# Kernel optimization log

Measured on AMD Instinct MI355X. Metric: run time of the kernel, lower is better.

## Reference

```python
import jax, jax.numpy as jnp
import numpy as np

H = 256
K = 16
EPS_LN = 1e-5


def setup_inputs() -> dict:
    key = jax.random.key(0)
    ks = jax.random.split(key, 24)
    B, N = 64, 256
    s = lambda *sh: 1.0 / np.sqrt(sh[0])
    inp = {
        "feat": jax.random.normal(ks[0], (B, N, H), jnp.float32),
        "centers": jax.random.normal(ks[1], (B, N, 3), jnp.float32),
        "text_global": jax.random.normal(ks[2], (B, H), jnp.float32),
        # geom_mlp: Linear(4,H) -> ReLU -> Linear(H,H) -> ReLU
        "w_geom1": jax.random.normal(ks[3], (4, H), jnp.float32) * s(4),
        "b_geom1": jnp.zeros((H,), jnp.float32),
        "w_geom2": jax.random.normal(ks[4], (H, H), jnp.float32) * s(H),
        "b_geom2": jnp.zeros((H,), jnp.float32),
        # text gate / bias projections
        "w_gate": jax.random.normal(ks[5], (H, H), jnp.float32) * s(H),
        "b_gate": jnp.zeros((H,), jnp.float32),
        "w_tbias": jax.random.normal(ks[6], (H, H), jnp.float32) * s(H),
        "b_tbias": jnp.zeros((H,), jnp.float32),
        # edge_mlp: Linear(H,H//2) -> ReLU -> Linear(H//2,1)
        "w_edge1": jax.random.normal(ks[7], (H, H // 2), jnp.float32) * s(H),
        "b_edge1": jnp.zeros((H // 2,), jnp.float32),
        "w_edge2": jax.random.normal(ks[8], (H // 2, 1), jnp.float32) * s(H // 2),
        "b_edge2": jnp.zeros((1,), jnp.float32),
        # msg_mlp: Linear(H,H) -> ReLU
        "w_msg": jax.random.normal(ks[9], (H, H), jnp.float32) * s(H),
        "b_msg": jnp.zeros((H,), jnp.float32),
        # out_proj: Linear(2H,H) -> ReLU
        "w_out": jax.random.normal(ks[10], (2 * H, H), jnp.float32) * s(2 * H),
        "b_out": jnp.zeros((H,), jnp.float32),
        # LayerNorm params
        "ln_gamma": jnp.ones((H,), jnp.float32),
        "ln_beta": jnp.zeros((H,), jnp.float32),
    }
    return inp


def _forward(feat, centers, text_global,
             w_geom1, b_geom1, w_geom2, b_geom2,
             w_gate, b_gate, w_tbias, b_tbias,
             w_edge1, b_edge1, w_edge2, b_edge2,
             w_msg, b_msg, w_out, b_out, ln_gamma, ln_beta):
    B, N, Hd = feat.shape
    k = min(K, N)
    # pairwise euclidean distances (B,N,N)
    sq = jnp.sum(centers * centers, axis=-1)  # (B,N)
    d2 = sq[:, :, None] + sq[:, None, :] - 2.0 * jnp.einsum('bnc,bmc->bnm', centers, centers)
    dist_matrix = jnp.sqrt(jnp.maximum(d2, 0.0))
    # k smallest -> top_k of negated distances (sorted ascending in distance)
    _, knn_idx = jax.lax.top_k(-dist_matrix, k)  # (B,N,k)
    idx_flat = knn_idx.reshape(B, N * k)
    feat_neigh = jnp.take_along_axis(feat, idx_flat[:, :, None], axis=1).reshape(B, N, k, Hd)
    centers_neigh = jnp.take_along_axis(centers, idx_flat[:, :, None], axis=1).reshape(B, N, k, 3)
    rel = centers_neigh - centers[:, :, None, :]  # (B,N,k,3)
    dist = jnp.linalg.norm(rel, axis=-1, keepdims=True) + 1e-6
    geom = jnp.concatenate([rel, jnp.log1p(dist)], axis=-1)  # (B,N,k,4)
    geom_emb = jax.nn.relu(jax.nn.relu(geom @ w_geom1 + b_geom1) @ w_geom2 + b_geom2)
    text_gate = jax.nn.sigmoid(text_global @ w_gate + b_gate)[:, None, None, :]
    text_bias = (text_global @ w_tbias + b_tbias)[:, None, None, :]
    geom_cond = geom_emb * text_gate + text_bias
    edge_feat = jnp.tanh(feat[:, :, None, :] + feat_neigh + geom_cond)  # (B,N,k,H)
    edge_logits = (jax.nn.relu(edge_feat @ w_edge1 + b_edge1) @ w_edge2 + b_edge2)[..., 0]
    edge_alpha = jax.nn.softmax(edge_logits, axis=-1)[..., None]  # (B,N,k,1)
    msg = jax.nn.relu(feat_neigh @ w_msg + b_msg)
    ctx = jnp.sum(edge_alpha * msg, axis=2)  # (B,N,H)
    out = jax.nn.relu(jnp.concatenate([feat, ctx], axis=-1) @ w_out + b_out)
    x = feat + out
    mu = jnp.mean(x, axis=-1, keepdims=True)
    var = jnp.mean((x - mu) ** 2, axis=-1, keepdims=True)
    return (x - mu) / jnp.sqrt(var + EPS_LN) * ln_gamma + ln_beta


def reference(feat, centers, text_global,
              w_geom1, b_geom1, w_geom2, b_geom2,
              w_gate, b_gate, w_tbias, b_tbias,
              w_edge1, b_edge1, w_edge2, b_edge2,
              w_msg, b_msg, w_out, b_out, ln_gamma, ln_beta):
    return _forward(feat, centers, text_global,
                    w_geom1, b_geom1, w_geom2, b_geom2,
                    w_gate, b_gate, w_tbias, b_tbias,
                    w_edge1, b_edge1, w_edge2, b_edge2,
                    w_msg, b_msg, w_out, b_out, ln_gamma, ln_beta)
```

## Files before the change

kernel.cpp:

```cpp
#include <hip/hip_runtime.h>
#include <hip/hip_bf16.h>

#define H 256
#define KNN 16
#define NPT 256
#define BB 64

typedef unsigned short u16;
typedef unsigned int u32;
typedef __attribute__((ext_vector_type(8))) short shortx8;
typedef __attribute__((ext_vector_type(4))) float floatx4;

__device__ __forceinline__ u16 f2b(float f) {
    return __builtin_bit_cast(u16, __float2bfloat16(f));
}
__device__ __forceinline__ float b2f(u16 u) {
    return __uint_as_float(((u32)u) << 16);
}

__device__ __forceinline__ float fast_tanh(float x) {
    float e = __builtin_amdgcn_exp2f(x * 2.88539008177793f);
    return 1.0f - 2.0f * __builtin_amdgcn_rcpf(e + 1.0f);
}

__global__ __launch_bounds__(256) void prep_kernel(
    const float* __restrict__ w2, const float* __restrict__ we1,
    const float* __restrict__ wm, const float* __restrict__ wo,
    const float* __restrict__ w1, const float* __restrict__ b1,
    u16* __restrict__ w2t, u16* __restrict__ we1t,
    u16* __restrict__ wmt, u16* __restrict__ wot, u16* __restrict__ w1t) {
    int tid = blockIdx.x * 256 + threadIdx.x;
    if (tid < 65536) {
        int n = tid >> 8, k = tid & 255;
        w2t[tid] = f2b(w2[k * 256 + n]);
    } else if (tid < 98304) {
        int t = tid - 65536;
        int n = t >> 8, k = t & 255;
        we1t[t] = f2b(we1[k * 128 + n]);
    } else if (tid < 163840) {
        int t = tid - 98304;
        int n = t >> 8, k = t & 255;
        wmt[t] = f2b(wm[k * 256 + n]);
    } else if (tid < 294912) {
        int t = tid - 163840;
        int n = t >> 9, k = t & 511;
        wot[t] = f2b(wo[k * 256 + n]);
    } else {
        int t = tid - 294912;
        int n = t >> 5, k = t & 31;
        float v = (k < 4) ? w1[k * 256 + n] : (k == 4 ? b1[n] : 0.0f);
        w1t[t] = f2b(v);
    }
}

__global__ __launch_bounds__(256) void knn_kernel(const float* __restrict__ centers,
                                                  int* __restrict__ knn) {
    __shared__ float cx[NPT], cy[NPT], cz[NPT], sq[NPT];
    __shared__ float dl[4][64][17];
    __shared__ int il[4][64][17];
    int blk = blockIdx.x;
    int b = blk >> 2, n0 = (blk & 3) * 64;
    int h = threadIdx.x;
    int s = h >> 6, pt = h & 63;
    {
        const float* cb = centers + (size_t)b * NPT * 3;
        float x = cb[h * 3 + 0], y = cb[h * 3 + 1], z = cb[h * 3 + 2];
        cx[h] = x; cy[h] = y; cz[h] = z;
        sq[h] = x * x + y * y + z * z;
    }
    __syncthreads();
    int n = n0 + pt;
    float x = cx[n], y = cy[n], z = cz[n], sn = sq[n];
    float bd[KNN];
    int bi[KNN];
#pragma unroll
    for (int j = 0; j < KNN; j++) { bd[j] = 1e30f; bi[j] = 0x7fffffff; }
    for (int mm = 0; mm < 64; mm++) {
        int m = s * 64 + mm;
        float dot = x * cx[m] + y * cy[m] + z * cz[m];
        float d2 = (sn + sq[m]) - 2.0f * dot;
        float d = sqrtf(fmaxf(d2, 0.0f));
        if (d < bd[KNN - 1]) {
            bd[KNN - 1] = d; bi[KNN - 1] = m;
#pragma unroll
            for (int p = KNN - 1; p > 0; --p) {
                if (bd[p - 1] > bd[p]) {
                    float td = bd[p - 1]; bd[p - 1] = bd[p]; bd[p] = td;
                    int ti = bi[p - 1]; bi[p - 1] = bi[p]; bi[p] = ti;
                }
            }
        }
    }
#pragma unroll
    for (int j = 0; j < KNN; j++) { dl[s][pt][j] = bd[j]; il[s][pt][j] = bi[j]; }
    __syncthreads();
    if (s == 0) {
        float md[KNN];
        int mi[KNN];
#pragma unroll
        for (int j = 0; j < KNN; j++) { md[j] = dl[0][pt][j]; mi[j] = il[0][pt][j]; }
        for (int t = 1; t < 4; t++) {
            for (int j = 0; j < KNN; j++) {
                float d = dl[t][pt][j];
                int idx = il[t][pt][j];
                bool ins = (d < md[KNN - 1]) || (d == md[KNN - 1] && idx < mi[KNN - 1]);
                if (!ins) break;
                md[KNN - 1] = d; mi[KNN - 1] = idx;
#pragma unroll
                for (int p = KNN - 1; p > 0; --p) {
                    bool sw = (md[p - 1] > md[p]) ||
                              (md[p - 1] == md[p] && mi[p - 1] > mi[p]);
                    if (sw) {
                        float td = md[p - 1]; md[p - 1] = md[p]; md[p] = td;
                        int ti = mi[p - 1]; mi[p - 1] = mi[p]; mi[p] = ti;
                    }
                }
            }
        }
        int* kp = knn + (b * NPT + n0 + pt) * KNN;
#pragma unroll
        for (int j = 0; j < KNN; j++) kp[j] = mi[j];
    }
}

__global__ __launch_bounds__(1024) void gate_kernel(const float* __restrict__ tg_g,
                                                    const float* __restrict__ wg,
                                                    const float* __restrict__ bg,
                                                    const float* __restrict__ wtb,
                                                    const float* __restrict__ btb,
                                                    float* __restrict__ gate,
                                                    float* __restrict__ tbias) {
    __shared__ float tg[H];
    __shared__ float red[1024];
    int b = blockIdx.x, t = threadIdx.x;
    if (t < H) tg[t] = tg_g[b * H + t];
    __syncthreads();
    int o = t & 511;
    int half = t >> 9;
    int h = o & 255;
    const float* wsel = (o < 256) ? wg : wtb;
    float a = 0.0f;
#pragma unroll 4
    for (int i = half * 128; i < half * 128 + 128; i++)
        a += tg[i] * wsel[i * H + h];
    red[t] = a;
    __syncthreads();
    if (t < 512) {
        float s = red[t] + red[t + 512];
        if (o < 256) {
            gate[b * H + h] = 1.0f / (1.0f + expf(-(s + bg[h])));
        } else {
            tbias[b * H + h] = s + btb[h];
        }
    }
}

__global__ __launch_bounds__(256, 4) void msg_mfma(const float* __restrict__ feat,
                                                   const u16* __restrict__ wmt,
                                                   const float* __restrict__ bm,
                                                   u16* __restrict__ MSGB) {
    __shared__ __attribute__((aligned(16))) u16 A[64][264];
    int p0 = blockIdx.x * 64, h = threadIdx.x;
    int w = h >> 6, lane = h & 63, quad = lane >> 4, lq = lane & 15;
#pragma unroll 8
    for (int row = 0; row < 64; row++)
        A[row][h] = f2b(feat[(size_t)(p0 + row) * H + h]);
    __syncthreads();
    floatx4 acc[4][4];
#pragma unroll
    for (int rt = 0; rt < 4; rt++)
#pragma unroll
        for (int ct = 0; ct < 4; ct++) acc[rt][ct] = (floatx4){0, 0, 0, 0};
#pragma unroll 2
    for (int kt = 0; kt < 8; kt++) {
        shortx8 bf[4];
#pragma unroll
        for (int ct = 0; ct < 4; ct++)
            bf[ct] = *(const shortx8*)&wmt[(w * 64 + ct * 16 + lq) * 256 + kt * 32 + quad * 8];
#pragma unroll
        for (int rt = 0; rt < 4; rt++) {
            shortx8 a = *(const shortx8*)&A[rt * 16 + lq][kt * 32 + quad * 8];
#pragma unroll
            for (int ct = 0; ct < 4; ct++)
                acc[rt][ct] = __builtin_amdgcn_mfma_f32_16x16x32_bf16(a, bf[ct], acc[rt][ct], 0, 0, 0);
        }
    }
#pragma unroll
    for (int ct = 0; ct < 4; ct++) {
        int col = w * 64 + ct * 16 + lq;
        float bmc = bm[col];
#pragma unroll
        for (int rt = 0; rt < 4; rt++)
#pragma unroll
            for (int r = 0; r < 4; r++) {
                int row = rt * 16 + quad * 4 + r;
                MSGB[(size_t)(p0 + row) * H + col] = f2b(fmaxf(acc[rt][ct][r] + bmc, 0.0f));
            }
    }
}

__global__ __launch_bounds__(256, 4) void edge_mfma(
    const float* __restrict__ feat,
    const float* __restrict__ centers,
    const u16* __restrict__ w1t,
    const u16* __restrict__ w2t, const float* __restrict__ b2v,
    const u16* __restrict__ we1t, const float* __restrict__ be1,
    const float* __restrict__ we2, const float* __restrict__ be2,
    const int* __restrict__ knn, const float* __restrict__ gateG,
    const float* __restrict__ tbiasG, const u16* __restrict__ MSGB,
    u16* __restrict__ ctxB) {
    __shared__ __attribute__((aligned(16))) u16 A[64][264];
    __shared__ float fnS[4][H];
    __shared__ __attribute__((aligned(16))) float geomS[64][4];
    __shared__ int nidxS[64];
    __shared__ float part[4][64];
    __shared__ float logitsS[64];
    __shared__ float alphaS[64];

    int bn0 = blockIdx.x * 4;
    int b = bn0 >> 8, n0 = bn0 & 255;
    int h = threadIdx.x;
    int w = h >> 6, lane = h & 63, quad = lane >> 4, lq = lane & 15;

    if (h < 64) nidxS[h] = knn[bn0 * KNN + h];
#pragma unroll
    for (int p = 0; p < 4; p++)
        fnS[p][h] = feat[(size_t)(bn0 + p) * H + h];
    if (h < 64) {
        int p = h >> 4;
        int m = nidxS[h];
        int n = n0 + p;
        const float* cb = centers + (size_t)b * NPT * 3;
        float rx = cb[m * 3 + 0] - cb[n * 3 + 0];
        float ry = cb[m * 3 + 1] - cb[n * 3 + 1];
        float rz = cb[m * 3 + 2] - cb[n * 3 + 2];
        float dist = sqrtf(rx * rx + ry * ry + rz * rz) + 1e-6f;
        geomS[h][0] = rx; geomS[h][1] = ry; geomS[h][2] = rz;
        geomS[h][3] = log1pf(dist);
    }
    __syncthreads();

    {
        shortx8 bw1[4];
#pragma unroll
        for (int ct = 0; ct < 4; ct++)
            bw1[ct] = *(const shortx8*)&w1t[(w * 64 + ct * 16 + lq) * 32 + quad * 8];
#pragma unroll
        for (int rt = 0; rt < 4; rt++) {
            shortx8 ag = {0, 0, 0, 0, 0, 0, 0, 0};
            if (quad == 0) {
                float4 g = *(const float4*)&geomS[rt * 16 + lq][0];
                ag[0] = (short)f2b(g.x);
                ag[1] = (short)f2b(g.y);
                ag[2] = (short)f2b(g.z);
                ag[3] = (short)f2b(g.w);
                ag[4] = (short)0x3F80;
            }
#pragma unroll
            for (int ct = 0; ct < 4; ct++) {
                floatx4 accg = __builtin_amdgcn_mfma_f32_16x16x32_bf16(
                    ag, bw1[ct], (floatx4){0, 0, 0, 0}, 0, 0, 0);
#pragma unroll
                for (int r = 0; r < 4; r++)
                    A[rt * 16 + quad * 4 + r][w * 64 + ct * 16 + lq] =
                        f2b(fmaxf(accg[r], 0.0f));
            }
        }
    }
    __syncthreads();

    floatx4 acc[4][4];
#pragma unroll
    for (int rt = 0; rt < 4; rt++)
#pragma unroll
        for (int ct = 0; ct < 4; ct++) acc[rt][ct] = (floatx4){0, 0, 0, 0};
    __builtin_amdgcn_s_setprio(1);
#pragma unroll 2
    for (int kt = 0; kt < 8; kt++) {
        shortx8 bf[4];
#pragma unroll
        for (int ct = 0; ct < 4; ct++)
            bf[ct] = *(const shortx8*)&w2t[(w * 64 + ct * 16 + lq) * 256 + kt * 32 + quad * 8];
#pragma unroll
        for (int rt = 0; rt < 4; rt++) {
            shortx8 a = *(const shortx8*)&A[rt * 16 + lq][kt * 32 + quad * 8];
#pragma unroll
            for (int ct = 0; ct < 4; ct++)
                acc[rt][ct] = __builtin_amdgcn_mfma_f32_16x16x32_bf16(a, bf[ct], acc[rt][ct], 0, 0, 0);
        }
    }
    __builtin_amdgcn_s_setprio(0);
    __syncthreads();

    {
        float b2c4[4], gc4[4], tc4[4];
#pragma unroll
        for (int ct = 0; ct < 4; ct++) {
            int col = w * 64 + ct * 16 + lq;
            b2c4[ct] = b2v[col];
            gc4[ct]  = gateG[b * H + col];
            tc4[ct]  = tbiasG[b * H + col];
        }
#pragma unroll
        for (int rt = 0; rt < 4; rt++) {
            float fnt4[4];
#pragma unroll
            for (int ct = 0; ct < 4; ct++)
                fnt4[ct] = fnS[rt][w * 64 + ct * 16 + lq] + tc4[ct];
#pragma unroll
            for (int r = 0; r < 4; r++) {
                int row = rt * 16 + quad * 4 + r;
                const float* rowp = feat + ((size_t)b * NPT + nidxS[row]) * H + w * 64 + lq;
#pragma unroll
                for (int ct = 0; ct < 4; ct++) {
                    float fb = rowp[ct * 16];
                    float emb = fmaxf(acc[rt][ct][r] + b2c4[ct], 0.0f);
                    A[row][w * 64 + ct * 16 + lq] = f2b(fast_tanh(fnt4[ct] + fb + emb * gc4[ct]));
                }
            }
        }
    }
    __syncthreads();

    floatx4 acc2[4][2];
#pragma unroll
    for (int rt = 0; rt < 4; rt++)
#pragma unroll
        for (int c2 = 0; c2 < 2; c2++) acc2[rt][c2] = (floatx4){0, 0, 0, 0};
    __builtin_amdgcn_s_setprio(1);
#pragma unroll 2
    for (int kt = 0; kt < 8; kt++) {
        shortx8 bf[2];
#pragma unroll
        for (int c2 = 0; c2 < 2; c2++)
            bf[c2] = *(const shortx8*)&we1t[(w * 32 + c2 * 16 + lq) * 256 + kt * 32 + quad * 8];
#pragma unroll
        for (int rt = 0; rt < 4; rt++) {
            shortx8 a = *(const shortx8*)&A[rt * 16 + lq][kt * 32 + quad * 8];
#pragma unroll
            for (int c2 = 0; c2 < 2; c2++)
                acc2[rt][c2] = __builtin_amdgcn_mfma_f32_16x16x32_bf16(a, bf[c2], acc2[rt][c2], 0, 0, 0);
        }
    }
    __builtin_amdgcn_s_setprio(0);

    float pl[4][4];
#pragma unroll
    for (int rt = 0; rt < 4; rt++)
#pragma unroll
        for (int r = 0; r < 4; r++) pl[rt][r] = 0.0f;
#pragma unroll
    for (int c2 = 0; c2 < 2; c2++) {
        int col = w * 32 + c2 * 16 + lq;
        float be1c = be1[col], w2c = we2[col];
#pragma unroll
        for (int rt = 0; rt < 4; rt++)
#pragma unroll
            for (int r = 0; r < 4; r++)
                pl[rt][r] += fmaxf(acc2[rt][c2][r] + be1c, 0.0f) * w2c;
    }
#pragma unroll
    for (int d = 1; d < 16; d <<= 1)
#pragma unroll
        for (int rt = 0; rt < 4; rt++)
#pragma unroll
            for (int r = 0; r < 4; r++) pl[rt][r] += __shfl_xor(pl[rt][r], d, 16);
    if (lq == 0) {
#pragma unroll
        for (int rt = 0; rt < 4; rt++)
#pragma unroll
            for (int r = 0; r < 4; r++)
                part[w][rt * 16 + quad * 4 + r] = pl[rt][r];
    }
    __syncthreads();
    if (h < 64)
        logitsS[h] = part[0][h] + part[1][h] + part[2][h] + part[3][h] + be2[0];
    __syncthreads();
    if (h < 64) {
        int base = (h >> 4) * 16;
        float mx = -1e30f;
#pragma unroll
        for (int j = 0; j < KNN; j++) mx = fmaxf(mx, logitsS[base + j]);
        float sum = 0.0f;
#pragma unroll
        for (int j = 0; j < KNN; j++) sum += expf(logitsS[base + j] - mx);
        alphaS[h] = expf(logitsS[h] - mx) / sum;
    }
    __syncthreads();

    {
        int p = h >> 6, cg = (h & 63) * 4;
        float4 c = {0, 0, 0, 0};
#pragma unroll
        for (int j = 0; j < KNN; j++) {
            float al = alphaS[p * 16 + j];
            const u32* mp = (const u32*)&MSGB[((size_t)b * NPT + nidxS[p * 16 + j]) * H + cg];
            u32 m0 = mp[0], m1 = mp[1];
            c.x += al * __uint_as_float(m0 << 16);
            c.y += al * __uint_as_float(m0 & 0xFFFF0000u);
            c.z += al * __uint_as_float(m1 << 16);
            c.w += al * __uint_as_float(m1 & 0xFFFF0000u);
        }
        uint2 st;
        st.x = (u32)f2b(c.x) | ((u32)f2b(c.y) << 16);
        st.y = (u32)f2b(c.z) | ((u32)f2b(c.w) << 16);
        *(uint2*)&ctxB[(size_t)(bn0 + p) * H + cg] = st;
    }
}

__global__ __launch_bounds__(256, 4) void out_mfma(const float* __restrict__ feat,
                                                   const u16* __restrict__ ctxB,
                                                   const u16* __restrict__ wot,
                                                   const float* __restrict__ bo,
                                                   const float* __restrict__ gamma,
                                                   const float* __restrict__ beta,
                                                   float* __restrict__ out) {
    __shared__ __attribute__((aligned(16))) u16 A[32][520];
    __shared__ float redS[4][32], redS2[4][32];
    int p0 = blockIdx.x * 32, h = threadIdx.x;
    int w = h >> 6, lane = h & 63, quad = lane >> 4, lq = lane & 15;
#pragma unroll 8
    for (int row = 0; row < 32; row++) {
        A[row][h]       = f2b(feat[(size_t)(p0 + row) * H + h]);
        A[row][256 + h] = ctxB[(size_t)(p0 + row) * H + h];
    }
    __syncthreads();
    floatx4 acc[2][4];
#pragma unroll
    for (int rt = 0; rt < 2; rt++)
#pragma unroll
        for (int ct = 0; ct < 4; ct++) acc[rt][ct] = (floatx4){0, 0, 0, 0};
#pragma unroll 2
    for (int kt = 0; kt < 16; kt++) {
        shortx8 bf[4];
#pragma unroll
        for (int ct = 0; ct < 4; ct++)
            bf[ct] = *(const shortx8*)&wot[(w * 64 + ct * 16 + lq) * 512 + kt * 32 + quad * 8];
#pragma unroll
        for (int rt = 0; rt < 2; rt++) {
            shortx8 a = *(const shortx8*)&A[rt * 16 + lq][kt * 32 + quad * 8];
#pragma unroll
            for (int ct = 0; ct < 4; ct++)
                acc[rt][ct] = __builtin_amdgcn_mfma_f32_16x16x32_bf16(a, bf[ct], acc[rt][ct], 0, 0, 0);
        }
    }
    float x[2][4][4];
    float sm[2][4], sq2[2][4];
#pragma unroll
    for (int rt = 0; rt < 2; rt++)
#pragma unroll
        for (int r = 0; r < 4; r++) { sm[rt][r] = 0.0f; sq2[rt][r] = 0.0f; }
#pragma unroll
    for (int rt = 0; rt < 2; rt++)
#pragma unroll
        for (int ct = 0; ct < 4; ct++) {
            int col = w * 64 + ct * 16 + lq;
            float boc = bo[col];
#pragma unroll
            for (int r = 0; r < 4; r++) {
                int row = rt * 16 + quad * 4 + r;
                float xx = feat[(size_t)(p0 + row) * H + col] +
                           fmaxf(acc[rt][ct][r] + boc, 0.0f);
                x[rt][ct][r] = xx;
                sm[rt][r] += xx;
                sq2[rt][r] += xx * xx;
            }
        }
#pragma unroll
    for (int d = 1; d < 16; d <<= 1)
#pragma unroll
        for (int rt = 0; rt < 2; rt++)
#pragma unroll
            for (int r = 0; r < 4; r++) {
                sm[rt][r] += __shfl_xor(sm[rt][r], d, 16);
                sq2[rt][r] += __shfl_xor(sq2[rt][r], d, 16);
            }
    if (lq == 0) {
#pragma unroll
        for (int rt = 0; rt < 2; rt++)
#pragma unroll
            for (int r = 0; r < 4; r++) {
                redS[w][rt * 16 + quad * 4 + r] = sm[rt][r];
                redS2[w][rt * 16 + quad * 4 + r] = sq2[rt][r];
            }
    }
    __syncthreads();
#pragma unroll
    for (int rt = 0; rt < 2; rt++)
#pragma unroll
        for (int r = 0; r < 4; r++) {
            int row = rt * 16 + quad * 4 + r;
            float s1 = redS[0][row] + redS[1][row] + redS[2][row] + redS[3][row];
            float s2 = redS2[0][row] + redS2[1][row] + redS2[2][row] + redS2[3][row];
            float mu = s1 * (1.0f / H);
            float var = s2 * (1.0f / H) - mu * mu;
            float inv = rsqrtf(fmaxf(var, 0.0f) + 1e-5f);
#pragma unroll
            for (int ct = 0; ct < 4; ct++) {
                int col = w * 64 + ct * 16 + lq;
                out[(size_t)(p0 + row) * H + col] =
                    (x[rt][ct][r] - mu) * inv * gamma[col] + beta[col];
            }
        }
}

extern "C" void kernel_launch(void* const* d_in, const int* in_sizes, int n_in,
                              void* d_out, int out_size, void* d_ws, size_t ws_size,
                              hipStream_t stream) {
    const float* feat    = (const float*)d_in[0];
    const float* centers = (const float*)d_in[1];
    const float* textg   = (const float*)d_in[2];
    const float* w1      = (const float*)d_in[3];
    const float* b1      = (const float*)d_in[4];
    const float* w2      = (const float*)d_in[5];
    const float* b2      = (const float*)d_in[6];
    const float* wg      = (const float*)d_in[7];
    const float* bg      = (const float*)d_in[8];
    const float* wtb     = (const float*)d_in[9];
    const float* btb     = (const float*)d_in[10];
    const float* we1     = (const float*)d_in[11];
    const float* be1     = (const float*)d_in[12];
    const float* we2     = (const float*)d_in[13];
    const float* be2     = (const float*)d_in[14];
    const float* wm      = (const float*)d_in[15];
    const float* bm      = (const float*)d_in[16];
    const float* wo      = (const float*)d_in[17];
    const float* bo      = (const float*)d_in[18];
    const float* gamma   = (const float*)d_in[19];
    const float* beta    = (const float*)d_in[20];

    char* ws = (char*)d_ws;
    size_t off = 0;
    int* knn     = (int*)(ws + off);   off += (size_t)BB * NPT * KNN * 4;
    float* gate  = (float*)(ws + off); off += (size_t)BB * H * 4;
    float* tbias = (float*)(ws + off); off += (size_t)BB * H * 4;
    u16* MSGB    = (u16*)(ws + off);   off += (size_t)BB * NPT * H * 2;
    u16* ctxB    = (u16*)(ws + off);   off += (size_t)BB * NPT * H * 2;
    u16* w2t     = (u16*)(ws + off);   off += (size_t)256 * 256 * 2;
    u16* we1t    = (u16*)(ws + off);   off += (size_t)128 * 256 * 2;
    u16* wmt     = (u16*)(ws + off);   off += (size_t)256 * 256 * 2;
    u16* wot     = (u16*)(ws + off);   off += (size_t)256 * 512 * 2;
    u16* w1t     = (u16*)(ws + off);   off += (size_t)256 * 32 * 2;

    prep_kernel<<<1184, 256, 0, stream>>>(w2, we1, wm, wo, w1, b1,
                                          w2t, we1t, wmt, wot, w1t);
    knn_kernel<<<256, 256, 0, stream>>>(centers, knn);
    gate_kernel<<<BB, 1024, 0, stream>>>(textg, wg, bg, wtb, btb, gate, tbias);
    msg_mfma<<<BB * NPT / 64, 256, 0, stream>>>(feat, wmt, bm, MSGB);
    edge_mfma<<<BB * NPT / 4, 256, 0, stream>>>(feat, centers, w1t, w2t, b2,
                                                we1t, be1, we2, be2, knn, gate, tbias,
                                                MSGB, ctxB);
    out_mfma<<<BB * NPT / 32, 256, 0, stream>>>(feat, ctxB, wot, bo,
                                                gamma, beta, (float*)d_out);
}
```

Measured before the change: 336.2 us.

## Tile weight transpose through shared memory and remap edge block order across XCDs

The weight-prep kernel now transposes 64x64 tiles through padded shared memory, so both the fp32 reads and the bf16 writes are coalesced instead of strided. It runs on 73 blocks instead of 1184. The edge kernel also remaps blockIdx so consecutive hardware block IDs map to different contiguous regions, which likely groups neighbouring batch points on the same XCD for L2 locality of gathered neighbour data. The trade-off is fewer, longer prep blocks, and the benefit of the remap depends on the dispatch pattern.

```diff
diff --git a/kernel.cpp b/kernel.cpp
--- a/kernel.cpp
+++ b/kernel.cpp
@@ -29,27 +29,32 @@
     const float* __restrict__ w1, const float* __restrict__ b1,
     u16* __restrict__ w2t, u16* __restrict__ we1t,
     u16* __restrict__ wmt, u16* __restrict__ wot, u16* __restrict__ w1t) {
-    int tid = blockIdx.x * 256 + threadIdx.x;
-    if (tid < 65536) {
-        int n = tid >> 8, k = tid & 255;
-        w2t[tid] = f2b(w2[k * 256 + n]);
-    } else if (tid < 98304) {
-        int t = tid - 65536;
-        int n = t >> 8, k = t & 255;
-        we1t[t] = f2b(we1[k * 128 + n]);
-    } else if (tid < 163840) {
-        int t = tid - 98304;
-        int n = t >> 8, k = t & 255;
-        wmt[t] = f2b(wm[k * 256 + n]);
-    } else if (tid < 294912) {
-        int t = tid - 163840;
-        int n = t >> 9, k = t & 511;
-        wot[t] = f2b(wo[k * 256 + n]);
-    } else {
-        int t = tid - 294912;
-        int n = t >> 5, k = t & 31;
-        float v = (k < 4) ? w1[k * 256 + n] : (k == 4 ? b1[n] : 0.0f);
-        w1t[t] = f2b(v);
+    int bid = blockIdx.x, t = threadIdx.x;
+    if (bid == 72) {
+        for (int e = t; e < 8192; e += 256) {
+            int n = e >> 5, k = e & 31;
+            float v = (k < 4) ? w1[k * 256 + n] : (k == 4 ? b1[n] : 0.0f);
+            w1t[e] = f2b(v);
+        }
+        return;
+    }
+    const float* in; u16* outp; int K, N, kt, nt;
+    if (bid < 16)      { in = w2;  outp = w2t;  K = 256; N = 256; int q = bid;      kt = q >> 2; nt = q & 3; }
+    else if (bid < 24) { in = we1; outp = we1t; K = 256; N = 128; int q = bid - 16; kt = q >> 1; nt = q & 1; }
+    else if (bid < 40) { in = wm;  outp = wmt;  K = 256; N = 256; int q = bid - 24; kt = q >> 2; nt = q & 3; }
+    else               { in = wo;  outp = wot;  K = 512; N = 256; int q = bid - 40; kt = q >> 2; nt = q & 3; }
+    __shared__ u16 T[64][66];
+    int c = t & 63, r0 = t >> 6;
+#pragma unroll
+    for (int i = 0; i < 16; i++) {
+        int r = r0 + i * 4;
+        T[r][c] = f2b(in[(size_t)(kt * 64 + r) * N + nt * 64 + c]);
+    }
+    __syncthreads();
+#pragma unroll
+    for (int i = 0; i < 16; i++) {
+        int r = r0 + i * 4;
+        outp[(size_t)(nt * 64 + r) * K + kt * 64 + c] = T[c][r];
     }
 }
 
@@ -217,7 +222,8 @@
     __shared__ float logitsS[64];
     __shared__ float alphaS[64];
 
-    int bn0 = blockIdx.x * 4;
+    int wid = (blockIdx.x & 7) * 512 + (blockIdx.x >> 3);
+    int bn0 = wid * 4;
     int b = bn0 >> 8, n0 = bn0 & 255;
     int h = threadIdx.x;
     int w = h >> 6, lane = h & 63, quad = lane >> 4, lq = lane & 15;
@@ -542,8 +548,8 @@
     u16* wot     = (u16*)(ws + off);   off += (size_t)256 * 512 * 2;
     u16* w1t     = (u16*)(ws + off);   off += (size_t)256 * 32 * 2;
 
-    prep_kernel<<<1184, 256, 0, stream>>>(w2, we1, wm, wo, w1, b1,
-                                          w2t, we1t, wmt, wot, w1t);
+    prep_kernel<<<73, 256, 0, stream>>>(w2, we1, wm, wo, w1, b1,
+                                        w2t, we1t, wmt, wot, w1t);
     knn_kernel<<<256, 256, 0, stream>>>(centers, knn);
     gate_kernel<<<BB, 1024, 0, stream>>>(textg, wg, bg, wtb, btb, gate, tbias);
     msg_mfma<<<BB * NPT / 64, 256, 0, stream>>>(feat, wmt, bm, MSGB);
```

After: 342.0 us. No clear change (+1.7%).
